# Kernel optimization log

Measured on AMD Instinct MI355X. Metric: run time of the kernel, lower is better.

## Reference

```python
import jax, jax.numpy as jnp
import numpy as np

H = 256
EPS = 1e-5
WIN = (-2, -1, 1, 2)  # radius_graph(pos/2^(d+1), k=2) on unit-spaced timestamps


def leaky(x):
    return jnp.where(x >= 0, x, 0.2 * x)


def layernorm(x, g, b):
    mu = jnp.mean(x, axis=-1, keepdims=True)
    var = jnp.mean(jnp.square(x - mu), axis=-1, keepdims=True)
    return (x - mu) * jax.lax.rsqrt(var + EPS) * g + b


def nbr_mean(x, offsets):
    # mean over temporal-window neighbors within each video row; [B,T,C]
    if not offsets:
        return jnp.zeros_like(x)
    T = x.shape[1]
    idx = jnp.arange(T)
    acc = jnp.zeros_like(x)
    cnt = jnp.zeros((T,), x.dtype)
    for o in offsets:
        valid = (idx + o >= 0) & (idx + o < T)
        acc = acc + jnp.where(valid[None, :, None], jnp.roll(x, -o, axis=1), 0.0)
        cnt = cnt + valid.astype(x.dtype)
    return acc / jnp.maximum(cnt, 1.0)[None, :, None]


def conv(x, Ws, Wn, b, offsets):
    # GraphConv with mean aggregation: W_self x_i + W_nbr mean_j x_j + b
    return x @ Ws + nbr_mean(x, offsets) @ Wn + b


def stage(x, s, Wself, Wnbr, bconv, ln_g, ln_b, offsets):
    # Dropout(eval)=id; conv; LeakyReLU(0.2); conv; LayerNorm; LeakyReLU(0.2)
    x = leaky(conv(x, Wself[s, 0], Wnbr[s, 0], bconv[s, 0], offsets))
    x = conv(x, Wself[s, 1], Wnbr[s, 1], bconv[s, 1], offsets)
    return leaky(layernorm(x, ln_g[s], ln_b[s]))


def upsample2(c):
    # knn_interpolate(k=2) from coarse (stride-2 subsampled) grid back to fine grid:
    # even fine nodes coincide with a coarse node (dist 0 -> weight ~inf -> copy);
    # odd fine nodes are equidistant from two coarse nodes (0.5/0.5), except the
    # last odd node whose 2-NN are at dist s and 3s -> weights 0.9/0.1.
    even = c
    nxt = jnp.concatenate([c[:, 1:], c[:, -1:]], axis=1)
    odd = 0.5 * (c + nxt)
    odd = odd.at[:, -1].set(0.9 * c[:, -1] + 0.1 * c[:, -2])
    B, Tc, C = c.shape
    return jnp.stack([even, odd], axis=2).reshape(B, 2 * Tc, C)


def setup_inputs() -> dict:
    key = jax.random.key(0)
    ks = jax.random.split(key, 8)
    B, T, F = 16, 4096, 1024
    N = B * T
    x = jax.random.normal(ks[0], (N, 1, F), dtype=jnp.float32)
    pos = (jnp.arange(N) % T).astype(jnp.float32)
    batch = (jnp.arange(N) // T).astype(jnp.int64)
    indices = (jnp.arange(N) % T).astype(jnp.int64)
    Wp = jax.random.normal(ks[1], (F, H), dtype=jnp.float32) / np.sqrt(F)
    bp = jnp.zeros((H,), jnp.float32)
    Wself = jax.random.normal(ks[2], (6, 2, H, H), dtype=jnp.float32) / np.sqrt(H)
    Wnbr = jax.random.normal(ks[3], (6, 2, H, H), dtype=jnp.float32) / np.sqrt(H)
    bconv = jnp.zeros((6, 2, H), jnp.float32)
    ln_g = jnp.ones((6, H), jnp.float32)
    ln_b = jnp.zeros((6, H), jnp.float32)
    return {"x": x, "pos": pos, "batch": batch, "indices": indices, "B": B, "T": T,
            "Wp": Wp, "bp": bp, "Wself": Wself, "Wnbr": Wnbr, "bconv": bconv,
            "ln_g": ln_g, "ln_b": ln_b}


def reference(x, pos, batch, indices, B, T, Wp, bp, Wself, Wnbr, bconv, ln_g, ln_b):
    # input projection: Rearrange 'B S F -> B (S F)' (S=1) + Linear
    feat = x.reshape(B, T, -1) @ Wp + bp  # [B,T,H]
    # ---- Temporal Encoder ----
    f = feat
    skips = [feat]  # depth-0 input graph features
    for d in range(3):
        f = f[:, ::2]  # batch_subsampling time pooling (stride 2)
        f = f + stage(f, d, Wself, Wnbr, bconv, ln_g, ln_b, WIN)
        if d < 2:
            skips.append(f)
    # ---- Function-Aware Decoder (eval path: clustering_at_inference=False) ----
    for i in range(3):
        res = skips[2 - i]
        f = res + upsample2(f)  # knn_interpolate(k=2) + skip
        dep = 2 - i
        # radius_graph(indices, 1.5): pooled index spacing 2^dep > 1.5 for dep>=1 -> no edges
        offs = WIN if dep == 0 else ()
        f = stage(f, 3 + i, Wself, Wnbr, bconv, ln_g, ln_b, offs)
    return f  # finest-resolution decoder output [B,T,H]
```

## Files before the change

kernel.cpp:

```cpp
#include <hip/hip_runtime.h>

#define HH 256

typedef __attribute__((ext_vector_type(8))) short short8;
typedef __attribute__((ext_vector_type(4))) float f32x4;
typedef __attribute__((ext_vector_type(4))) unsigned short u16x4;
typedef __attribute__((ext_vector_type(8))) unsigned short u16x8;

constexpr int NBATCH = 16;
constexpr int T0   = 4096;
constexpr int FDIM = 1024;
constexpr int R0   = NBATCH * T0;
constexpr int R1   = R0 / 2;
constexpr int R2   = R0 / 4;
constexpr int R3   = R0 / 8;

__device__ __forceinline__ float b2f(unsigned short u) {
    union { unsigned int i; float f; } v; v.i = ((unsigned int)u) << 16; return v.f;
}
__device__ __forceinline__ unsigned short f2b(float f) {
    union { float f; unsigned int i; } v; v.f = f;
    unsigned int r = v.i + 0x7fffu + ((v.i >> 16) & 1u);
    return (unsigned short)(r >> 16);
}
__device__ __forceinline__ void gload16(const void* g, void* l) {
    __builtin_amdgcn_global_load_lds((const __attribute__((address_space(1))) void*)g,
                                     (__attribute__((address_space(3))) void*)l, 16, 0, 0);
}
__device__ __forceinline__ int swz_ks(int chunk)        { return (chunk & 3) ^ ((chunk >> 3) & 3); }
__device__ __forceinline__ int frag_idx(int row, int g) { return (row * 4 + (g ^ ((row >> 1) & 3))) * 8; }

__global__ void transpose_w(const float* __restrict__ src, unsigned short* __restrict__ dst,
                            int K, int tilesPerMat)
{
    int bid = blockIdx.x;
    int m = bid / tilesPerMat;
    int t = bid % tilesPerMat;
    int tr = t >> 3, tc = t & 7;
    const float* S = src + (size_t)m * K * HH;
    unsigned short* D = dst + (size_t)m * HH * K;
    __shared__ float tile[32][33];
    int x = threadIdx.x & 31, y = threadIdx.x >> 5;
#pragma unroll
    for (int i = y; i < 32; i += 8)
        tile[i][x] = S[(size_t)(tr * 32 + i) * HH + tc * 32 + x];
    __syncthreads();
#pragma unroll
    for (int i = y; i < 32; i += 8)
        D[(size_t)(tc * 32 + i) * K + tr * 32 + x] = f2b(tile[x][i]);
}

template<int AMODE, int NBR, int LEAKY>
__launch_bounds__(512)
__global__ void conv_gemm(const unsigned short* __restrict__ A,
                          const unsigned short* __restrict__ Cc,
                          const unsigned short* __restrict__ Bself,
                          const unsigned short* __restrict__ Bnbr,
                          const float* __restrict__ bias,
                          unsigned short* __restrict__ out,
                          int Tl, int Tc, int tlshift)
{
    __shared__ unsigned short As[2][128 * 32];
    __shared__ unsigned short Bs[2][256 * 32];
    const int tid  = threadIdx.x;
    const int lane = tid & 63;
    const int w    = tid >> 6;
    const int wm   = w & 1, wn = w >> 1;
    const long row0 = (long)blockIdx.x * 128;

    const int arr = tid >> 2;
    const int akk = swz_ks(tid);
    const long gr = row0 + arr;

    float ca = 0.f, cb = 0.f; size_t rc0 = 0, rc1 = 0;
    if (AMODE == 2) {
        int t = (int)(gr & (long)(Tl - 1));
        long bq = gr >> tlshift;
        int k = t >> 1;
        rc0 = (size_t)bq * Tc + k;
        if (!(t & 1))        { ca = 1.0f; cb = 0.0f; rc1 = rc0; }
        else if (k < Tc - 1) { ca = 0.5f; cb = 0.5f; rc1 = rc0 + 1; }
        else                 { ca = 0.9f; cb = 0.1f; rc1 = rc0 - 1; }
    }
    int vmask = 0; float vinv = 1.f;
    size_t nrow0 = 0, nrow1 = 0, nrow2 = 0, nrow3 = 0;
    if (NBR) {
        const int offs[4] = {-2, -1, 1, 2};
        int t = (int)(gr & (long)(Tl - 1));
        int cnt = 0;
        size_t nr[4] = {0, 0, 0, 0};
#pragma unroll
        for (int oi = 0; oi < 4; oi++) {
            int tn = t + offs[oi];
            if (tn >= 0 && tn < Tl) {
                vmask |= 1 << oi; cnt++;
                long r = gr + offs[oi];
                nr[oi] = (size_t)((AMODE == 1) ? 2 * r : r) * HH;
            }
        }
        vinv = 1.f / (float)cnt;
        nrow0 = nr[0]; nrow1 = nr[1]; nrow2 = nr[2]; nrow3 = nr[3];
    }

    f32x4 acc[4][4] = {};
    u16x8 pv0 = {}, pv1 = {}, pv2 = {}, pv3 = {};

    const int NT = NBR ? 16 : 8;

    auto issue = [&](int t, int b) {
        const int seg = NBR ? (t >> 3) : 0;
        const int k0 = (t & 7) * 32;
        const unsigned short* __restrict__ Bm = (NBR && seg) ? Bnbr : Bself;
        gload16(Bm + (size_t)arr * HH + k0 + akk * 8,        &Bs[b][tid * 8]);
        gload16(Bm + (size_t)(128 + arr) * HH + k0 + akk * 8, &Bs[b][(tid + 512) * 8]);
        if (seg == 0) {
            if (AMODE == 0) {
                gload16(A + (size_t)gr * HH + k0 + akk * 8, &As[b][tid * 8]);
            } else if (AMODE == 1) {
                gload16(A + (size_t)(2 * gr) * HH + k0 + akk * 8, &As[b][tid * 8]);
            } else {
                pv0 = *(const u16x8*)(A + (size_t)gr * HH + k0 + akk * 8);
                pv1 = *(const u16x8*)(Cc + rc0 * HH + k0 + akk * 8);
                pv2 = *(const u16x8*)(Cc + rc1 * HH + k0 + akk * 8);
            }
        } else {
            if (vmask & 1) pv0 = *(const u16x8*)(A + nrow0 + k0 + akk * 8);
            if (vmask & 2) pv1 = *(const u16x8*)(A + nrow1 + k0 + akk * 8);
            if (vmask & 4) pv2 = *(const u16x8*)(A + nrow2 + k0 + akk * 8);
            if (vmask & 8) pv3 = *(const u16x8*)(A + nrow3 + k0 + akk * 8);
        }
    };
    auto finish = [&](int t, int b) {
        const int seg = NBR ? (t >> 3) : 0;
        if (seg == 0) {
            if (AMODE == 2) {
                u16x8 o;
#pragma unroll
                for (int j = 0; j < 8; j++)
                    o[j] = f2b(b2f(pv0[j]) + ca * b2f(pv1[j]) + cb * b2f(pv2[j]));
                *(u16x8*)&As[b][tid * 8] = o;
            }
        } else {
            float a8[8] = {0, 0, 0, 0, 0, 0, 0, 0};
            if (vmask & 1) {
#pragma unroll
                for (int j = 0; j < 8; j++) a8[j] += b2f(pv0[j]);
            }
            if (vmask & 2) {
#pragma unroll
                for (int j = 0; j < 8; j++) a8[j] += b2f(pv1[j]);
            }
            if (vmask & 4) {
#pragma unroll
                for (int j = 0; j < 8; j++) a8[j] += b2f(pv2[j]);
            }
            if (vmask & 8) {
#pragma unroll
                for (int j = 0; j < 8; j++) a8[j] += b2f(pv3[j]);
            }
            u16x8 o;
#pragma unroll
            for (int j = 0; j < 8; j++) o[j] = f2b(a8[j] * vinv);
            *(u16x8*)&As[b][tid * 8] = o;
        }
    };

    issue(0, 0);
    finish(0, 0);
    __syncthreads();

    int buf = 0;
#pragma unroll
    for (int t = 0; t < NT; ++t) {
        if (t + 1 < NT) issue(t + 1, buf ^ 1);

        short8 af[4], bg[4];
#pragma unroll
        for (int i = 0; i < 4; i++) {
            af[i] = *(const short8*)&As[buf][frag_idx(wm * 64 + i * 16 + (lane & 15), lane >> 4)];
            bg[i] = *(const short8*)&Bs[buf][frag_idx(wn * 64 + i * 16 + (lane & 15), lane >> 4)];
        }
#pragma unroll
        for (int mi = 0; mi < 4; mi++)
#pragma unroll
            for (int ni = 0; ni < 4; ni++)
                acc[mi][ni] = __builtin_amdgcn_mfma_f32_16x16x32_bf16(af[mi], bg[ni], acc[mi][ni], 0, 0, 0);

        if (t + 1 < NT) {
            finish(t + 1, buf ^ 1);
            __syncthreads();
            buf ^= 1;
        }
    }

#pragma unroll
    for (int mi = 0; mi < 4; mi++) {
        size_t rbase = (size_t)row0 + wm * 64 + mi * 16 + (lane >> 4) * 4;
#pragma unroll
        for (int ni = 0; ni < 4; ni++) {
            int c = wn * 64 + ni * 16 + (lane & 15);
            float bb = bias[c];
            f32x4 v = acc[mi][ni];
#pragma unroll
            for (int r = 0; r < 4; r++) {
                float t = v[r] + bb;
                if (LEAKY) t = (t >= 0.f) ? t : 0.2f * t;
                out[(rbase + r) * HH + c] = f2b(t);
            }
        }
    }
}

__launch_bounds__(512)
__global__ void proj_gemm(const float* __restrict__ A, const unsigned short* __restrict__ Bt,
                          const float* __restrict__ bias, unsigned short* __restrict__ out)
{
    __shared__ unsigned short As[2][128 * 32];
    __shared__ unsigned short Bs[2][256 * 32];
    const int tid  = threadIdx.x;
    const int lane = tid & 63;
    const int w    = tid >> 6;
    const int wm   = w & 1, wn = w >> 1;
    const size_t row0 = (size_t)blockIdx.x * 128;

    const int arr = tid >> 2;
    const int akk = swz_ks(tid);

    f32x4 acc[4][4] = {};
    float4 pa0, pa1;

    const int NT = FDIM / 32;

    auto issue = [&](int t, int b) {
        const int k0 = t * 32;
        gload16(Bt + (size_t)arr * FDIM + k0 + akk * 8,         &Bs[b][tid * 8]);
        gload16(Bt + (size_t)(128 + arr) * FDIM + k0 + akk * 8, &Bs[b][(tid + 512) * 8]);
        const float* s = A + (row0 + arr) * (size_t)FDIM + k0 + akk * 8;
        pa0 = *(const float4*)s;
        pa1 = *(const float4*)(s + 4);
    };
    auto finish = [&](int t, int b) {
        u16x8 o = { f2b(pa0.x), f2b(pa0.y), f2b(pa0.z), f2b(pa0.w),
                    f2b(pa1.x), f2b(pa1.y), f2b(pa1.z), f2b(pa1.w) };
        *(u16x8*)&As[b][tid * 8] = o;
    };

    issue(0, 0);
    finish(0, 0);
    __syncthreads();

    int buf = 0;
    for (int t = 0; t < NT; ++t) {
        if (t + 1 < NT) issue(t + 1, buf ^ 1);

        short8 af[4], bg[4];
#pragma unroll
        for (int i = 0; i < 4; i++) {
            af[i] = *(const short8*)&As[buf][frag_idx(wm * 64 + i * 16 + (lane & 15), lane >> 4)];
            bg[i] = *(const short8*)&Bs[buf][frag_idx(wn * 64 + i * 16 + (lane & 15), lane >> 4)];
        }
#pragma unroll
        for (int mi = 0; mi < 4; mi++)
#pragma unroll
            for (int ni = 0; ni < 4; ni++)
                acc[mi][ni] = __builtin_amdgcn_mfma_f32_16x16x32_bf16(af[mi], bg[ni], acc[mi][ni], 0, 0, 0);

        if (t + 1 < NT) {
            finish(t + 1, buf ^ 1);
            __syncthreads();
            buf ^= 1;
        }
    }

#pragma unroll
    for (int mi = 0; mi < 4; mi++) {
        size_t rbase = row0 + wm * 64 + mi * 16 + (lane >> 4) * 4;
#pragma unroll
        for (int ni = 0; ni < 4; ni++) {
            int c = wn * 64 + ni * 16 + (lane & 15);
            float bb = bias[c];
            f32x4 v = acc[mi][ni];
#pragma unroll
            for (int r = 0; r < 4; r++)
                out[(rbase + r) * HH + c] = f2b(v[r] + bb);
        }
    }
}

__global__ void upsample_add_kernel(unsigned short* __restrict__ res, const unsigned short* __restrict__ c,
                                    int Tc, int tlshift, int Rout)
{
    int idx = blockIdx.x * 256 + threadIdx.x;
    int r = idx >> 5, cc = (idx & 31) * 8;
    if (r >= Rout) return;
    int Tl = Tc * 2;
    int t  = r & (Tl - 1);
    int bq = r >> tlshift;
    int k  = t >> 1;
    size_t rc = (size_t)bq * Tc + k;
    float u[8];
    if (!(t & 1)) {
        u16x8 v = *(const u16x8*)(c + rc * HH + cc);
#pragma unroll
        for (int j = 0; j < 8; j++) u[j] = b2f(v[j]);
    } else if (k < Tc - 1) {
        u16x8 v0 = *(const u16x8*)(c + rc * HH + cc);
        u16x8 v1 = *(const u16x8*)(c + (rc + 1) * HH + cc);
#pragma unroll
        for (int j = 0; j < 8; j++) u[j] = 0.5f * (b2f(v0[j]) + b2f(v1[j]));
    } else {
        u16x8 v0 = *(const u16x8*)(c + rc * HH + cc);
        u16x8 vm = *(const u16x8*)(c + (rc - 1) * HH + cc);
#pragma unroll
        for (int j = 0; j < 8; j++) u[j] = 0.9f * b2f(v0[j]) + 0.1f * b2f(vm[j]);
    }
    u16x8 rv = *(const u16x8*)(res + (size_t)r * HH + cc);
    u16x8 o;
#pragma unroll
    for (int j = 0; j < 8; j++) o[j] = f2b(b2f(rv[j]) + u[j]);
    *(u16x8*)(res + (size_t)r * HH + cc) = o;
}

template<int MODE>
__launch_bounds__(256)
__global__ void ln_kernel(const unsigned short* __restrict__ src, void* __restrict__ dstv,
                          const unsigned short* __restrict__ prev,
                          const float* __restrict__ g, const float* __restrict__ b)
{
    size_t row = (size_t)blockIdx.x * 4 + (threadIdx.x >> 6);
    int lane = threadIdx.x & 63;
    u16x4 xv = *(const u16x4*)(src + row * HH + lane * 4);
    float x0 = b2f(xv[0]), x1 = b2f(xv[1]), x2 = b2f(xv[2]), x3 = b2f(xv[3]);

    float s = x0 + x1 + x2 + x3;
#pragma unroll
    for (int off = 32; off >= 1; off >>= 1) s += __shfl_xor(s, off);
    float mu = s * (1.0f / HH);

    float d0 = x0 - mu, d1 = x1 - mu, d2 = x2 - mu, d3 = x3 - mu;
    float vs = d0 * d0 + d1 * d1 + d2 * d2 + d3 * d3;
#pragma unroll
    for (int off = 32; off >= 1; off >>= 1) vs += __shfl_xor(vs, off);
    float inv = rsqrtf(vs * (1.0f / HH) + 1e-5f);

    float4 gv = *reinterpret_cast<const float4*>(g + lane * 4);
    float4 bv = *reinterpret_cast<const float4*>(b + lane * 4);
    float y0 = d0 * inv * gv.x + bv.x;
    float y1 = d1 * inv * gv.y + bv.y;
    float y2 = d2 * inv * gv.z + bv.z;
    float y3 = d3 * inv * gv.w + bv.w;
    y0 = (y0 >= 0.f) ? y0 : 0.2f * y0;
    y1 = (y1 >= 0.f) ? y1 : 0.2f * y1;
    y2 = (y2 >= 0.f) ? y2 : 0.2f * y2;
    y3 = (y3 >= 0.f) ? y3 : 0.2f * y3;

    if (MODE == 2) {
        float* d = (float*)dstv + row * HH + lane * 4;
        *reinterpret_cast<float4*>(d) = make_float4(y0, y1, y2, y3);
    } else {
        if (MODE == 1) {
            u16x4 rv = *(const u16x4*)(prev + (2 * row) * HH + lane * 4);
            y0 += b2f(rv[0]); y1 += b2f(rv[1]); y2 += b2f(rv[2]); y3 += b2f(rv[3]);
        }
        unsigned short* d = (unsigned short*)dstv + row * HH + lane * 4;
        u16x4 o = { f2b(y0), f2b(y1), f2b(y2), f2b(y3) };
        *(u16x4*)d = o;
    }
}

extern "C" void kernel_launch(void* const* d_in, const int* in_sizes, int n_in,
                              void* d_out, int out_size, void* d_ws, size_t ws_size,
                              hipStream_t stream)
{
    const float* x     = (const float*)d_in[0];
    const float* Wp    = (const float*)d_in[6];
    const float* bp    = (const float*)d_in[7];
    const float* Wself = (const float*)d_in[8];
    const float* Wnbr  = (const float*)d_in[9];
    const float* bconv = (const float*)d_in[10];
    const float* ln_g  = (const float*)d_in[11];
    const float* ln_b  = (const float*)d_in[12];
    float* out = (float*)d_out;

    char* p = (char*)d_ws;
    unsigned short* Wself_t = (unsigned short*)p; p += (size_t)12 * HH * HH * 2;
    unsigned short* Wnbr_t  = (unsigned short*)p; p += (size_t)12 * HH * HH * 2;
    unsigned short* Wp_t    = (unsigned short*)p; p += (size_t)HH * FDIM * 2;
    unsigned short* c0 = (unsigned short*)p; p += (size_t)R0 * HH * 2;
    unsigned short* c1 = (unsigned short*)p; p += (size_t)R1 * HH * 2;
    unsigned short* c2 = (unsigned short*)p; p += (size_t)R2 * HH * 2;
    unsigned short* c3 = (unsigned short*)p; p += (size_t)R3 * HH * 2;
    unsigned short* t1 = (unsigned short*)p; p += (size_t)R0 * HH * 2;
    unsigned short* t2 = (unsigned short*)p; p += (size_t)R0 * HH * 2;
    if (ws_size < (size_t)(p - (char*)d_ws)) return;

    auto Ws = [&](int i) { return Wself_t + (size_t)i * HH * HH; };
    auto Wn = [&](int i) { return Wnbr_t  + (size_t)i * HH * HH; };

    transpose_w<<<12 * 64, 256, 0, stream>>>(Wself, Wself_t, HH, 64);
    transpose_w<<<12 * 64, 256, 0, stream>>>(Wnbr,  Wnbr_t,  HH, 64);
    transpose_w<<<256, 256, 0, stream>>>(Wp, Wp_t, FDIM, 256);

    proj_gemm<<<R0 / 128, 512, 0, stream>>>(x, Wp_t, bp, c0);

    conv_gemm<1, 1, 1><<<R1 / 128, 512, 0, stream>>>(c0, nullptr, Ws(0), Wn(0), bconv + 0 * HH, t1, 2048, 0, 0);
    conv_gemm<0, 1, 0><<<R1 / 128, 512, 0, stream>>>(t1, nullptr, Ws(1), Wn(1), bconv + 1 * HH, t2, 2048, 0, 0);
    ln_kernel<1><<<R1 / 4, 256, 0, stream>>>(t2, c1, c0, ln_g + 0 * HH, ln_b + 0 * HH);

    conv_gemm<1, 1, 1><<<R2 / 128, 512, 0, stream>>>(c1, nullptr, Ws(2), Wn(2), bconv + 2 * HH, t1, 1024, 0, 0);
    conv_gemm<0, 1, 0><<<R2 / 128, 512, 0, stream>>>(t1, nullptr, Ws(3), Wn(3), bconv + 3 * HH, t2, 1024, 0, 0);
    ln_kernel<1><<<R2 / 4, 256, 0, stream>>>(t2, c2, c1, ln_g + 1 * HH, ln_b + 1 * HH);

    conv_gemm<1, 1, 1><<<R3 / 128, 512, 0, stream>>>(c2, nullptr, Ws(4), Wn(4), bconv + 4 * HH, t1, 512, 0, 0);
    conv_gemm<0, 1, 0><<<R3 / 128, 512, 0, stream>>>(t1, nullptr, Ws(5), Wn(5), bconv + 5 * HH, t2, 512, 0, 0);
    ln_kernel<1><<<R3 / 4, 256, 0, stream>>>(t2, c3, c2, ln_g + 2 * HH, ln_b + 2 * HH);

    conv_gemm<2, 0, 1><<<R2 / 128, 512, 0, stream>>>(c2, c3, Ws(6), nullptr, bconv + 6 * HH, t1, 1024, 512, 10);
    conv_gemm<0, 0, 0><<<R2 / 128, 512, 0, stream>>>(t1, nullptr, Ws(7), nullptr, bconv + 7 * HH, t2, 1024, 0, 0);
    ln_kernel<0><<<R2 / 4, 256, 0, stream>>>(t2, c2, nullptr, ln_g + 3 * HH, ln_b + 3 * HH);
    conv_gemm<2, 0, 1><<<R1 / 128, 512, 0, stream>>>(c1, c2, Ws(8), nullptr, bconv + 8 * HH, t1, 2048, 1024, 11);
    conv_gemm<0, 0, 0><<<R1 / 128, 512, 0, stream>>>(t1, nullptr, Ws(9), nullptr, bconv + 9 * HH, t2, 2048, 0, 0);
    ln_kernel<0><<<R1 / 4, 256, 0, stream>>>(t2, c1, nullptr, ln_g + 4 * HH, ln_b + 4 * HH);
    upsample_add_kernel<<<R0 / 8, 256, 0, stream>>>(c0, c1, 2048, 12, R0);
    conv_gemm<0, 1, 1><<<R0 / 128, 512, 0, stream>>>(c0, nullptr, Ws(10), Wn(10), bconv + 10 * HH, t1, 4096, 0, 0);
    conv_gemm<0, 1, 0><<<R0 / 128, 512, 0, stream>>>(t1, nullptr, Ws(11), Wn(11), bconv + 11 * HH, t2, 4096, 0, 0);
    ln_kernel<2><<<R0 / 4, 256, 0, stream>>>(t2, out, nullptr, ln_g + 5 * HH, ln_b + 5 * HH);
}
```

Measured before the change: 430.5 us.

## Fuse second graph-conv GEMM with LayerNorm, LeakyReLU and residual epilogue

Adds a conv2_ln kernel that runs the second GraphConv GEMM of each stage and then applies LayerNorm, LeakyReLU and the optional strided residual add in the epilogue. Row sums and sums of squares are reduced across the four column-warps through a small shared array. This removes the separate ln_kernel launches and the bf16 round-trip of the pre-norm activations through global memory. In exchange it uses the one-pass E[x^2]-mu^2 variance formula, which is less numerically stable, and LN now runs on unrounded fp32 accumulators rather than on bf16 values.

```diff
diff --git a/kernel.cpp b/kernel.cpp
--- a/kernel.cpp
+++ b/kernel.cpp
@@ -50,7 +50,7 @@
         D[(size_t)(tc * 32 + i) * K + tr * 32 + x] = f2b(tile[x][i]);
 }
 
-template<int AMODE, int NBR, int LEAKY>
+template<int AMODE, int NBR>
 __launch_bounds__(512)
 __global__ void conv_gemm(const unsigned short* __restrict__ A,
                           const unsigned short* __restrict__ Cc,
@@ -111,7 +111,7 @@
         const int seg = NBR ? (t >> 3) : 0;
         const int k0 = (t & 7) * 32;
         const unsigned short* __restrict__ Bm = (NBR && seg) ? Bnbr : Bself;
-        gload16(Bm + (size_t)arr * HH + k0 + akk * 8,        &Bs[b][tid * 8]);
+        gload16(Bm + (size_t)arr * HH + k0 + akk * 8,         &Bs[b][tid * 8]);
         gload16(Bm + (size_t)(128 + arr) * HH + k0 + akk * 8, &Bs[b][(tid + 512) * 8]);
         if (seg == 0) {
             if (AMODE == 0) {
@@ -204,8 +204,189 @@
 #pragma unroll
             for (int r = 0; r < 4; r++) {
                 float t = v[r] + bb;
-                if (LEAKY) t = (t >= 0.f) ? t : 0.2f * t;
+                t = (t >= 0.f) ? t : 0.2f * t;
                 out[(rbase + r) * HH + c] = f2b(t);
+            }
+        }
+    }
+}
+
+template<int NBR, int OUT>
+__launch_bounds__(512)
+__global__ void conv2_ln(const unsigned short* __restrict__ A,
+                         const unsigned short* __restrict__ prev,
+                         const unsigned short* __restrict__ Bself,
+                         const unsigned short* __restrict__ Bnbr,
+                         const float* __restrict__ bias,
+                         const float* __restrict__ lng,
+                         const float* __restrict__ lnb,
+                         void* __restrict__ dstv,
+                         int Tl)
+{
+    __shared__ unsigned short As[2][128 * 32];
+    __shared__ unsigned short Bs[2][256 * 32];
+    __shared__ float lnred[128][8];
+    const int tid  = threadIdx.x;
+    const int lane = tid & 63;
+    const int w    = tid >> 6;
+    const int wm   = w & 1, wn = w >> 1;
+    const long row0 = (long)blockIdx.x * 128;
+
+    const int arr = tid >> 2;
+    const int akk = swz_ks(tid);
+    const long gr = row0 + arr;
+
+    int vmask = 0; float vinv = 1.f;
+    size_t nrow0 = 0, nrow1 = 0, nrow2 = 0, nrow3 = 0;
+    if (NBR) {
+        const int offs[4] = {-2, -1, 1, 2};
+        int t = (int)(gr & (long)(Tl - 1));
+        int cnt = 0;
+        size_t nr[4] = {0, 0, 0, 0};
+#pragma unroll
+        for (int oi = 0; oi < 4; oi++) {
+            int tn = t + offs[oi];
+            if (tn >= 0 && tn < Tl) {
+                vmask |= 1 << oi; cnt++;
+                nr[oi] = (size_t)(gr + offs[oi]) * HH;
+            }
+        }
+        vinv = 1.f / (float)cnt;
+        nrow0 = nr[0]; nrow1 = nr[1]; nrow2 = nr[2]; nrow3 = nr[3];
+    }
+
+    f32x4 acc[4][4] = {};
+    u16x8 pv0 = {}, pv1 = {}, pv2 = {}, pv3 = {};
+
+    const int NT = NBR ? 16 : 8;
+
+    auto issue = [&](int t, int b) {
+        const int seg = NBR ? (t >> 3) : 0;
+        const int k0 = (t & 7) * 32;
+        const unsigned short* __restrict__ Bm = (NBR && seg) ? Bnbr : Bself;
+        gload16(Bm + (size_t)arr * HH + k0 + akk * 8,         &Bs[b][tid * 8]);
+        gload16(Bm + (size_t)(128 + arr) * HH + k0 + akk * 8, &Bs[b][(tid + 512) * 8]);
+        if (seg == 0) {
+            gload16(A + (size_t)gr * HH + k0 + akk * 8, &As[b][tid * 8]);
+        } else {
+            if (vmask & 1) pv0 = *(const u16x8*)(A + nrow0 + k0 + akk * 8);
+            if (vmask & 2) pv1 = *(const u16x8*)(A + nrow1 + k0 + akk * 8);
+            if (vmask & 4) pv2 = *(const u16x8*)(A + nrow2 + k0 + akk * 8);
+            if (vmask & 8) pv3 = *(const u16x8*)(A + nrow3 + k0 + akk * 8);
+        }
+    };
+    auto finish = [&](int t, int b) {
+        const int seg = NBR ? (t >> 3) : 0;
+        if (seg != 0) {
+            float a8[8] = {0, 0, 0, 0, 0, 0, 0, 0};
+            if (vmask & 1) {
+#pragma unroll
+                for (int j = 0; j < 8; j++) a8[j] += b2f(pv0[j]);
+            }
+            if (vmask & 2) {
+#pragma unroll
+                for (int j = 0; j < 8; j++) a8[j] += b2f(pv1[j]);
+            }
+            if (vmask & 4) {
+#pragma unroll
+                for (int j = 0; j < 8; j++) a8[j] += b2f(pv2[j]);
+            }
+            if (vmask & 8) {
+#pragma unroll
+                for (int j = 0; j < 8; j++) a8[j] += b2f(pv3[j]);
+            }
+            u16x8 o;
+#pragma unroll
+            for (int j = 0; j < 8; j++) o[j] = f2b(a8[j] * vinv);
+            *(u16x8*)&As[b][tid * 8] = o;
+        }
+    };
+
+    issue(0, 0);
+    finish(0, 0);
+    __syncthreads();
+
+    int buf = 0;
+#pragma unroll
+    for (int t = 0; t < NT; ++t) {
+        if (t + 1 < NT) issue(t + 1, buf ^ 1);
+
+        short8 af[4], bg[4];
+#pragma unroll
+        for (int i = 0; i < 4; i++) {
+            af[i] = *(const short8*)&As[buf][frag_idx(wm * 64 + i * 16 + (lane & 15), lane >> 4)];
+            bg[i] = *(const short8*)&Bs[buf][frag_idx(wn * 64 + i * 16 + (lane & 15), lane >> 4)];
+        }
+#pragma unroll
+        for (int mi = 0; mi < 4; mi++)
+#pragma unroll
+            for (int ni = 0; ni < 4; ni++)
+                acc[mi][ni] = __builtin_amdgcn_mfma_f32_16x16x32_bf16(af[mi], bg[ni], acc[mi][ni], 0, 0, 0);
+
+        if (t + 1 < NT) {
+            finish(t + 1, buf ^ 1);
+            __syncthreads();
+            buf ^= 1;
+        }
+    }
+
+    float bb[4];
+#pragma unroll
+    for (int ni = 0; ni < 4; ni++) bb[ni] = bias[wn * 64 + ni * 16 + (lane & 15)];
+
+#pragma unroll
+    for (int mi = 0; mi < 4; mi++) {
+#pragma unroll
+        for (int r = 0; r < 4; r++) {
+            float s = 0.f, q = 0.f;
+#pragma unroll
+            for (int ni = 0; ni < 4; ni++) {
+                float v = acc[mi][ni][r] + bb[ni];
+                s += v; q += v * v;
+            }
+            s += __shfl_xor(s, 1); q += __shfl_xor(q, 1);
+            s += __shfl_xor(s, 2); q += __shfl_xor(q, 2);
+            s += __shfl_xor(s, 4); q += __shfl_xor(q, 4);
+            s += __shfl_xor(s, 8); q += __shfl_xor(q, 8);
+            if ((lane & 15) == 0) {
+                int row = wm * 64 + mi * 16 + (lane >> 4) * 4 + r;
+                lnred[row][wn]     = s;
+                lnred[row][4 + wn] = q;
+            }
+        }
+    }
+    __syncthreads();
+
+    float gv[4], bv[4];
+#pragma unroll
+    for (int ni = 0; ni < 4; ni++) {
+        int c = wn * 64 + ni * 16 + (lane & 15);
+        gv[ni] = lng[c]; bv[ni] = lnb[c];
+    }
+
+#pragma unroll
+    for (int mi = 0; mi < 4; mi++) {
+#pragma unroll
+        for (int r = 0; r < 4; r++) {
+            int row = wm * 64 + mi * 16 + (lane >> 4) * 4 + r;
+            float s = lnred[row][0] + lnred[row][1] + lnred[row][2] + lnred[row][3];
+            float q = lnred[row][4] + lnred[row][5] + lnred[row][6] + lnred[row][7];
+            float mu  = s * (1.0f / HH);
+            float var = q * (1.0f / HH) - mu * mu;
+            float inv = rsqrtf(var + 1e-5f);
+            size_t grow = (size_t)row0 + row;
+#pragma unroll
+            for (int ni = 0; ni < 4; ni++) {
+                int c = wn * 64 + ni * 16 + (lane & 15);
+                float v = acc[mi][ni][r] + bb[ni];
+                float y = (v - mu) * inv * gv[ni] + bv[ni];
+                y = (y >= 0.f) ? y : 0.2f * y;
+                if (OUT == 2) {
+                    ((float*)dstv)[grow * HH + c] = y;
+                } else {
+                    if (OUT == 1) y += b2f(prev[(2 * grow) * HH + c]);
+                    ((unsigned short*)dstv)[grow * HH + c] = f2b(y);
+                }
             }
         }
     }
@@ -321,53 +502,6 @@
     *(u16x8*)(res + (size_t)r * HH + cc) = o;
 }
 
-template<int MODE>
-__launch_bounds__(256)
-__global__ void ln_kernel(const unsigned short* __restrict__ src, void* __restrict__ dstv,
-                          const unsigned short* __restrict__ prev,
-                          const float* __restrict__ g, const float* __restrict__ b)
-{
-    size_t row = (size_t)blockIdx.x * 4 + (threadIdx.x >> 6);
-    int lane = threadIdx.x & 63;
-    u16x4 xv = *(const u16x4*)(src + row * HH + lane * 4);
-    float x0 = b2f(xv[0]), x1 = b2f(xv[1]), x2 = b2f(xv[2]), x3 = b2f(xv[3]);
-
-    float s = x0 + x1 + x2 + x3;
-#pragma unroll
-    for (int off = 32; off >= 1; off >>= 1) s += __shfl_xor(s, off);
-    float mu = s * (1.0f / HH);
-
-    float d0 = x0 - mu, d1 = x1 - mu, d2 = x2 - mu, d3 = x3 - mu;
-    float vs = d0 * d0 + d1 * d1 + d2 * d2 + d3 * d3;
-#pragma unroll
-    for (int off = 32; off >= 1; off >>= 1) vs += __shfl_xor(vs, off);
-    float inv = rsqrtf(vs * (1.0f / HH) + 1e-5f);
-
-    float4 gv = *reinterpret_cast<const float4*>(g + lane * 4);
-    float4 bv = *reinterpret_cast<const float4*>(b + lane * 4);
-    float y0 = d0 * inv * gv.x + bv.x;
-    float y1 = d1 * inv * gv.y + bv.y;
-    float y2 = d2 * inv * gv.z + bv.z;
-    float y3 = d3 * inv * gv.w + bv.w;
-    y0 = (y0 >= 0.f) ? y0 : 0.2f * y0;
-    y1 = (y1 >= 0.f) ? y1 : 0.2f * y1;
-    y2 = (y2 >= 0.f) ? y2 : 0.2f * y2;
-    y3 = (y3 >= 0.f) ? y3 : 0.2f * y3;
-
-    if (MODE == 2) {
-        float* d = (float*)dstv + row * HH + lane * 4;
-        *reinterpret_cast<float4*>(d) = make_float4(y0, y1, y2, y3);
-    } else {
-        if (MODE == 1) {
-            u16x4 rv = *(const u16x4*)(prev + (2 * row) * HH + lane * 4);
-            y0 += b2f(rv[0]); y1 += b2f(rv[1]); y2 += b2f(rv[2]); y3 += b2f(rv[3]);
-        }
-        unsigned short* d = (unsigned short*)dstv + row * HH + lane * 4;
-        u16x4 o = { f2b(y0), f2b(y1), f2b(y2), f2b(y3) };
-        *(u16x4*)d = o;
-    }
-}
-
 extern "C" void kernel_launch(void* const* d_in, const int* in_sizes, int n_in,
                               void* d_out, int out_size, void* d_ws, size_t ws_size,
                               hipStream_t stream)
@@ -391,7 +525,6 @@
     unsigned short* c2 = (unsigned short*)p; p += (size_t)R2 * HH * 2;
     unsigned short* c3 = (unsigned short*)p; p += (size_t)R3 * HH * 2;
     unsigned short* t1 = (unsigned short*)p; p += (size_t)R0 * HH * 2;
-    unsigned short* t2 = (unsigned short*)p; p += (size_t)R0 * HH * 2;
     if (ws_size < (size_t)(p - (char*)d_ws)) return;
 
     auto Ws = [&](int i) { return Wself_t + (size_t)i * HH * HH; };
@@ -403,26 +536,26 @@
 
     proj_gemm<<<R0 / 128, 512, 0, stream>>>(x, Wp_t, bp, c0);
 
-    conv_gemm<1, 1, 1><<<R1 / 128, 512, 0, stream>>>(c0, nullptr, Ws(0), Wn(0), bconv + 0 * HH, t1, 2048, 0, 0);
-    conv_gemm<0, 1, 0><<<R1 / 128, 512, 0, stream>>>(t1, nullptr, Ws(1), Wn(1), bconv + 1 * HH, t2, 2048, 0, 0);
-    ln_kernel<1><<<R1 / 4, 256, 0, stream>>>(t2, c1, c0, ln_g + 0 * HH, ln_b + 0 * HH);
-
-    conv_gemm<1, 1, 1><<<R2 / 128, 512, 0, stream>>>(c1, nullptr, Ws(2), Wn(2), bconv + 2 * HH, t1, 1024, 0, 0);
-    conv_gemm<0, 1, 0><<<R2 / 128, 512, 0, stream>>>(t1, nullptr, Ws(3), Wn(3), bconv + 3 * HH, t2, 1024, 0, 0);
-    ln_kernel<1><<<R2 / 4, 256, 0, stream>>>(t2, c2, c1, ln_g + 1 * HH, ln_b + 1 * HH);
-
-    conv_gemm<1, 1, 1><<<R3 / 128, 512, 0, stream>>>(c2, nullptr, Ws(4), Wn(4), bconv + 4 * HH, t1, 512, 0, 0);
-    conv_gemm<0, 1, 0><<<R3 / 128, 512, 0, stream>>>(t1, nullptr, Ws(5), Wn(5), bconv + 5 * HH, t2, 512, 0, 0);
-    ln_kernel<1><<<R3 / 4, 256, 0, stream>>>(t2, c3, c2, ln_g + 2 * HH, ln_b + 2 * HH);
-
-    conv_gemm<2, 0, 1><<<R2 / 128, 512, 0, stream>>>(c2, c3, Ws(6), nullptr, bconv + 6 * HH, t1, 1024, 512, 10);
-    conv_gemm<0, 0, 0><<<R2 / 128, 512, 0, stream>>>(t1, nullptr, Ws(7), nullptr, bconv + 7 * HH, t2, 1024, 0, 0);
-    ln_kernel<0><<<R2 / 4, 256, 0, stream>>>(t2, c2, nullptr, ln_g + 3 * HH, ln_b + 3 * HH);
-    conv_gemm<2, 0, 1><<<R1 / 128, 512, 0, stream>>>(c1, c2, Ws(8), nullptr, bconv + 8 * HH, t1, 2048, 1024, 11);
-    conv_gemm<0, 0, 0><<<R1 / 128, 512, 0, stream>>>(t1, nullptr, Ws(9), nullptr, bconv + 9 * HH, t2, 2048, 0, 0);
-    ln_kernel<0><<<R1 / 4, 256, 0, stream>>>(t2, c1, nullptr, ln_g + 4 * HH, ln_b + 4 * HH);
+    conv_gemm<1, 1><<<R1 / 128, 512, 0, stream>>>(c0, nullptr, Ws(0), Wn(0), bconv + 0 * HH, t1, 2048, 0, 0);
+    conv2_ln<1, 1><<<R1 / 128, 512, 0, stream>>>(t1, c0, Ws(1), Wn(1), bconv + 1 * HH,
+                                                 ln_g + 0 * HH, ln_b + 0 * HH, c1, 2048);
+
+    conv_gemm<1, 1><<<R2 / 128, 512, 0, stream>>>(c1, nullptr, Ws(2), Wn(2), bconv + 2 * HH, t1, 1024, 0, 0);
+    conv2_ln<1, 1><<<R2 / 128, 512, 0, stream>>>(t1, c1, Ws(3), Wn(3), bconv + 3 * HH,
+                                                 ln_g + 1 * HH, ln_b + 1 * HH, c2, 1024);
+
+    conv_gemm<1, 1><<<R3 / 128, 512, 0, stream>>>(c2, nullptr, Ws(4), Wn(4), bconv + 4 * HH, t1, 512, 0, 0);
+    conv2_ln<1, 1><<<R3 / 128, 512, 0, stream>>>(t1, c2, Ws(5), Wn(5), bconv + 5 * HH,
+                                                 ln_g + 2 * HH, ln_b + 2 * HH, c3, 512);
+
+    conv_gemm<2, 0><<<R2 / 128, 512, 0, stream>>>(c2, c3, Ws(6), nullptr, bconv + 6 * HH, t1, 1024, 512, 10);
+    conv2_ln<0, 0><<<R2 / 128, 512, 0, stream>>>(t1, nullptr, Ws(7), nullptr, bconv + 7 * HH,
+                                                 ln_g + 3 * HH, ln_b + 3 * HH, c2, 1024);
+    conv_gemm<2, 0><<<R1 / 128, 512, 0, stream>>>(c1, c2, Ws(8), nullptr, bconv + 8 * HH, t1, 2048, 1024, 11);
+    conv2_ln<0, 0><<<R1 / 128, 512, 0, stream>>>(t1, nullptr, Ws(9), nullptr, bconv + 9 * HH,
+                                                 ln_g + 4 * HH, ln_b + 4 * HH, c1, 2048);
     upsample_add_kernel<<<R0 / 8, 256, 0, stream>>>(c0, c1, 2048, 12, R0);
-    conv_gemm<0, 1, 1><<<R0 / 128, 512, 0, stream>>>(c0, nullptr, Ws(10), Wn(10), bconv + 10 * HH, t1, 4096, 0, 0);
-    conv_gemm<0, 1, 0><<<R0 / 128, 512, 0, stream>>>(t1, nullptr, Ws(11), Wn(11), bconv + 11 * HH, t2, 4096, 0, 0);
-    ln_kernel<2><<<R0 / 4, 256, 0, stream>>>(t2, out, nullptr, ln_g + 5 * HH, ln_b + 5 * HH);
-}
+    conv_gemm<0, 1><<<R0 / 128, 512, 0, stream>>>(c0, nullptr, Ws(10), Wn(10), bconv + 10 * HH, t1, 4096, 0, 0);
+    conv2_ln<1, 2><<<R0 / 128, 512, 0, stream>>>(t1, nullptr, Ws(11), Wn(11), bconv + 11 * HH,
+                                                 ln_g + 5 * HH, ln_b + 5 * HH, out, 4096);
+}
```

Measured after the change: 395.1 us. 8.2% less time.
